# Kernel optimization log

Measured on AMD Instinct MI355X. Metric: run time of the kernel, lower is better.

## Reference

```python
import jax, jax.numpy as jnp
import numpy as np

HEADS = 8
CHANNELS = 256
RR = 1
DH = CHANNELS // RR                 # per-head channels
ATT = HEADS * DH                    # 2048
# exact scale from the torch module
SCALE = (1.0 / np.sqrt(CHANNELS // RR)) / np.sqrt(2.0 / (CHANNELS + 3 * ATT)) * np.sqrt(2.0 / (CHANNELS + ATT))


def setup_inputs() -> dict:
    key = jax.random.key(0)
    k1, k2, k3, k4, k5 = jax.random.split(key, 5)
    x = jax.random.normal(k1, (8, CHANNELS, 32, 32), dtype=jnp.float32)
    # 1x1 conv weights stored as [out_ch, in_ch]
    w_in = jax.random.normal(k2, (3 * ATT, CHANNELS), dtype=jnp.float32) * (1.0 / np.sqrt(CHANNELS))
    b_in = jax.random.normal(k3, (3 * ATT,), dtype=jnp.float32) * 0.02
    w_out = jax.random.normal(k4, (CHANNELS, ATT), dtype=jnp.float32) * (1.0 / np.sqrt(ATT))
    b_out = jax.random.normal(k5, (CHANNELS,), dtype=jnp.float32) * 0.02
    return {"x": x, "w_in": w_in, "b_in": b_in, "w_out": w_out, "b_out": b_out}


def reference(x, w_in, b_in, w_out, b_out):
    n, c, h, w = x.shape
    L = h * w
    xf = x.reshape(n, c, L)
    # 1x1 conv in = channel-mixing matmul, then fixed scale
    scaled = (jnp.einsum('ncl,oc->nol', xf, w_in) + b_in[:, None]) * jnp.float32(SCALE)
    s = scaled.reshape(n, HEADS, 3 * DH, L)
    q, k, v = s[:, :, :DH], s[:, :, DH:2 * DH], s[:, :, 2 * DH:]   # each (n, H, DH, L)
    att = jnp.einsum('nhdl,nhdm->nhlm', q, k)                       # (n, H, L, L)
    # softmax over the FLATTENED L*L axis (global per head), as in the torch code
    att = jax.nn.softmax(att.reshape(n, HEADS, L * L), axis=2).reshape(n, HEADS, L, L)
    out = jnp.einsum('nhdl,nhlm->nhdm', v, att)                     # (n, H, DH, L)
    out = out.reshape(n, ATT, L)
    out = jnp.einsum('nal,ca->ncl', out, w_out) + b_out[:, None]
    return out.reshape(n, c, h, w)
```

## Files before the change

### kernel.cpp

```cpp
#include <hip/hip_runtime.h>
#include <hip/hip_bf16.h>


typedef __bf16 bf16x8 __attribute__((ext_vector_type(8)));
typedef __bf16 bf16x4 __attribute__((ext_vector_type(4)));
typedef float f32x4 __attribute__((ext_vector_type(4)));
typedef __hip_bfloat16 bf16;

__device__ __forceinline__ void async_copy16(const void* g, void* s) {
    __builtin_amdgcn_global_load_lds(
        (const __attribute__((address_space(1))) unsigned int*)g,
        (__attribute__((address_space(3))) unsigned int*)s, 16, 0, 0);
}

__device__ __forceinline__ bf16x8 scale8(bf16x8 v, float s) {
    bf16x8 r;
#pragma unroll
    for (int e = 0; e < 8; ++e) r[e] = (__bf16)((float)v[e] * s);
    return r;
}

__global__ __launch_bounds__(256)
void gemm_nt(const bf16* __restrict__ A, const bf16* __restrict__ B, void* __restrict__ Cvoid,
             int M, int N, int K, int lda, int ldb, int ldc,
             long asn, long ash, long bsn, long bsh, long csn, long csh,
             int H, int mode, const float* __restrict__ bias, const float* __restrict__ Zp,
             float scale)
{
    __shared__ __align__(16) bf16 smem[17408];
    bf16* Alds = smem;
    bf16* Blds = smem + 8192;

    const int tid  = threadIdx.x;
    const int wave = tid >> 6;
    const int lane = tid & 63;
    const int z  = blockIdx.z;
    const int zn = z / H, zh = z % H;

    const bf16* Ab = A + zn * asn + zh * ash;
    const bf16* Bb = B + zn * bsn + zh * bsh;

    const long tM = (long)blockIdx.y * 128;
    const long tN = (long)blockIdx.x * 128;

    const int wr   = (wave >> 1) * 64;
    const int wc   = (wave & 1) * 64;
    const int l15  = lane & 15;
    const int quad = lane >> 4;

    f32x4 acc[4][4] = {};

    const int kiters = K >> 6;
    const bool regB = (mode == 4);

#pragma unroll
    for (int i = 0; i < 4; ++i) {
        const int flat = i * 256 + tid;
        const int row  = flat >> 3;
        const int kcs  = (flat & 7) ^ (row & 7);
        async_copy16(Ab + (tM + row) * (long)lda + kcs * 8,
                     (char*)Alds + (long)(i * 256 + wave * 64) * 16);
        if (!regB) {
            async_copy16(Bb + (tN + row) * (long)ldb + kcs * 8,
                         (char*)Blds + (long)(i * 256 + wave * 64) * 16);
        }
    }
    if (regB) {
        const float zi0 = 1.0f / Zp[zn * 8];
#pragma unroll
        for (int i = 0; i < 4; ++i) {
            const int flat = i * 256 + tid;
            const int row  = flat >> 3;
            const int kcs  = (flat & 7) ^ (row & 7);
            bf16x8 b = *(const bf16x8*)(Bb + (tN + row) * (long)ldb + kcs * 8);
            *(bf16x8*)((char*)Blds + (long)flat * 16) = scale8(b, zi0);
        }
    }

    bf16x8 pfA[4], pfB[4];
    for (int kt = 0; kt < kiters; ++kt) {
        __syncthreads();
        const bool has_next = (kt + 1 < kiters);
        float zin = 1.0f;
        if (has_next) {
            const long kof = (long)(kt + 1) * 64;
            if (regB) zin = 1.0f / Zp[zn * 8 + ((kt + 1) >> 2)];
#pragma unroll
            for (int i = 0; i < 4; ++i) {
                const int flat = i * 256 + tid;
                const int row  = flat >> 3;
                const int kcs  = (flat & 7) ^ (row & 7);
                pfA[i] = *(const bf16x8*)(Ab + (tM + row) * (long)lda + kof + kcs * 8);
                pfB[i] = *(const bf16x8*)(Bb + (tN + row) * (long)ldb + kof + kcs * 8);
            }
        }
#pragma unroll
        for (int kk = 0; kk < 2; ++kk) {
            bf16x8 af[4], bfv[4];
#pragma unroll
            for (int i = 0; i < 4; ++i) {
                const int r = wr + i * 16 + l15;
                af[i] = *(const bf16x8*)(Alds + r * 64 + ((kk * 4 + quad) ^ (r & 7)) * 8);
            }
#pragma unroll
            for (int j = 0; j < 4; ++j) {
                const int r = wc + j * 16 + l15;
                bfv[j] = *(const bf16x8*)(Blds + r * 64 + ((kk * 4 + quad) ^ (r & 7)) * 8);
            }
#pragma unroll
            for (int i = 0; i < 4; ++i)
#pragma unroll
                for (int j = 0; j < 4; ++j)
                    acc[i][j] = __builtin_amdgcn_mfma_f32_16x16x32_bf16(af[i], bfv[j], acc[i][j], 0, 0, 0);
        }
        if (has_next) {
            __builtin_amdgcn_sched_barrier(0);
            __builtin_amdgcn_s_barrier();
            __builtin_amdgcn_sched_barrier(0);
#pragma unroll
            for (int i = 0; i < 4; ++i) {
                const int flat = i * 256 + tid;
                *(bf16x8*)((char*)Alds + (long)flat * 16) = pfA[i];
                *(bf16x8*)((char*)Blds + (long)flat * 16) = regB ? scale8(pfB[i], zin) : pfB[i];
            }
        }
    }

    if (mode >= 3) {
        float* C = (float*)Cvoid + zn * csn + zh * csh;
#pragma unroll
        for (int i = 0; i < 4; ++i)
#pragma unroll
            for (int j = 0; j < 4; ++j)
#pragma unroll
                for (int r = 0; r < 4; ++r) {
                    const long row = tM + wr + i * 16 + quad * 4 + r;
                    const long col = tN + wc + j * 16 + l15;
                    C[row * (long)ldc + col] = acc[i][j][r] + bias[row];
                }
    } else {
        bf16* Cb = (bf16*)Cvoid + zn * csn + zh * csh + tM * (long)ldc + tN;
        __syncthreads();
#pragma unroll
        for (int i = 0; i < 4; ++i)
#pragma unroll
            for (int j = 0; j < 4; ++j)
#pragma unroll
                for (int r = 0; r < 4; ++r) {
                    const int row = wr + i * 16 + quad * 4 + r;
                    const int col = wc + j * 16 + l15;
                    smem[row * 136 + col] = __float2bfloat16((acc[i][j][r] + bias[col]) * scale);
                }
        __syncthreads();
#pragma unroll
        for (int k = 0; k < 8; ++k) {
            const int fc  = k * 256 + tid;
            const int row = fc >> 4, cc = fc & 15;
            const f32x4 val = *(const f32x4*)((const char*)smem + row * 272 + cc * 16);
            *(f32x4*)((char*)(Cb + (long)row * ldc) + cc * 16) = val;
        }
    }
}

__global__ __launch_bounds__(256, 2)
void attn_fused(const bf16* __restrict__ scaled_t, const bf16* __restrict__ v2,
                bf16* __restrict__ out_tt, float* __restrict__ Z)
{
    __shared__ __align__(16) bf16 smem[36880];
    bf16* Ks = smem;
    bf16* Qs = smem + 16384;
    bf16* Ps = smem + 32768;
    float* Zs = (float*)(smem + 36864);

    const int tid  = threadIdx.x;
    const int wave = tid >> 6, lane = tid & 63;
    const int l15  = lane & 15, quad = lane >> 4;

    const int b   = blockIdx.x;
    const int xcd = b & 7, s = b >> 3;
    const int nh  = xcd * 8 + (s >> 4);
    const int mt  = s & 15;
    const int n   = nh >> 3, h = nh & 7;
    const long m0 = (long)mt * 64;

    const bf16* Qb = scaled_t + (long)n * 6291456 + h * 768;
    const bf16* Kb = Qb + 256;
    const bf16* Vb = v2 + (long)nh * 262144;

    f32x4 accO[16] = {};
    float zsum = 0.0f;

#pragma unroll
    for (int i = 0; i < 8; ++i) {
        const int flat = i * 256 + tid;
        const int row  = flat >> 5;
        const int ch   = flat & 31;
        const int kcs  = (ch & 24) | ((ch & 7) ^ (row & 7));
        async_copy16(Kb + (m0 + row) * 6144 + kcs * 8,
                     (char*)Ks + (long)(i * 256 + wave * 64) * 16);
    }
    {
        bf16x8 q0[8];
#pragma unroll
        for (int i = 0; i < 8; ++i) {
            const int flat = i * 256 + tid;
            const int row  = flat >> 5;
            const int ch   = flat & 31;
            const int kcs  = (ch & 24) | ((ch & 7) ^ (row & 7));
            q0[i] = *(const bf16x8*)(Qb + (long)row * 6144 + kcs * 8);
        }
#pragma unroll
        for (int i = 0; i < 8; ++i)
            *(bf16x8*)((char*)Qs + (long)(i * 256 + tid) * 16) = q0[i];
    }
    __syncthreads();

    bf16x8 pfV[8], pfQ[8];
    for (int lt = 0; lt < 16; ++lt) {
        const long l0 = (long)lt * 64;

#pragma unroll
        for (int i = 0; i < 8; ++i) {
            const int flat = i * 256 + tid;
            const int d    = flat >> 3;
            const int kcs  = (flat & 7) ^ (d & 7);
            pfV[i] = *(const bf16x8*)(Vb + (long)d * 1024 + l0 + kcs * 8);
        }

        f32x4 accS[4] = {};
        const int qrow = wave * 16 + l15;
#pragma unroll
        for (int w = 0; w < 8; ++w) {
            const int cw = w * 4 + quad;
            const bf16x8 af = *(const bf16x8*)(
                Qs + qrow * 256 + ((cw & 24) | ((cw & 7) ^ (qrow & 7))) * 8);
#pragma unroll
            for (int j = 0; j < 4; ++j) {
                const int krow = j * 16 + l15;
                const bf16x8 bfv = *(const bf16x8*)(
                    Ks + krow * 256 + ((cw & 24) | ((cw & 7) ^ (krow & 7))) * 8);
                accS[j] = __builtin_amdgcn_mfma_f32_16x16x32_bf16(af, bfv, accS[j], 0, 0, 0);
            }
        }
        {
            const int lbase = wave * 16 + quad * 4;
            const int chunk = lbase >> 3;
#pragma unroll
            for (int j = 0; j < 4; ++j) {
                const int m = j * 16 + l15;
                float e0 = __expf(accS[j][0]);
                float e1 = __expf(accS[j][1]);
                float e2 = __expf(accS[j][2]);
                float e3 = __expf(accS[j][3]);
                zsum += (e0 + e1) + (e2 + e3);
                bf16x4 pk;
                pk[0] = (__bf16)e0; pk[1] = (__bf16)e1; pk[2] = (__bf16)e2; pk[3] = (__bf16)e3;
                *(bf16x4*)(Ps + m * 64 + (chunk ^ (m & 7)) * 8 + (lbase & 7)) = pk;
            }
        }
        __builtin_amdgcn_sched_barrier(0);
        __builtin_amdgcn_s_barrier();
        __builtin_amdgcn_sched_barrier(0);
#pragma unroll
        for (int i = 0; i < 8; ++i)
            *(bf16x8*)((char*)Qs + (long)(i * 256 + tid) * 16) = pfV[i];
        __syncthreads();

        if (lt < 15) {
            const long l0n = l0 + 64;
#pragma unroll
            for (int i = 0; i < 8; ++i) {
                const int flat = i * 256 + tid;
                const int row  = flat >> 5;
                const int ch   = flat & 31;
                const int kcs  = (ch & 24) | ((ch & 7) ^ (row & 7));
                pfQ[i] = *(const bf16x8*)(Qb + (l0n + row) * 6144 + kcs * 8);
            }
        }

        const int mrow = wave * 16 + l15;
#pragma unroll
        for (int w = 0; w < 2; ++w) {
            const int cw = w * 4 + quad;
            const bf16x8 af = *(const bf16x8*)(Ps + mrow * 64 + (cw ^ (mrow & 7)) * 8);
#pragma unroll
            for (int j = 0; j < 16; ++j) {
                const int d = j * 16 + l15;
                const bf16x8 bfv = *(const bf16x8*)(Qs + d * 64 + (cw ^ (d & 7)) * 8);
                accO[j] = __builtin_amdgcn_mfma_f32_16x16x32_bf16(af, bfv, accO[j], 0, 0, 0);
            }
        }
        __builtin_amdgcn_sched_barrier(0);
        __builtin_amdgcn_s_barrier();
        __builtin_amdgcn_sched_barrier(0);
        if (lt < 15) {
#pragma unroll
            for (int i = 0; i < 8; ++i)
                *(bf16x8*)((char*)Qs + (long)(i * 256 + tid) * 16) = pfQ[i];
        }
        __syncthreads();
    }

#pragma unroll
    for (int o = 32; o > 0; o >>= 1) zsum += __shfl_down(zsum, o);
    if (lane == 0) Zs[wave] = zsum;
    __syncthreads();
    if (tid == 0) atomicAdd(Z + nh, (Zs[0] + Zs[1]) + (Zs[2] + Zs[3]));

    bf16* Cs = smem + 16384;
#pragma unroll
    for (int j = 0; j < 16; ++j)
#pragma unroll
        for (int r = 0; r < 4; ++r) {
            const int row = wave * 16 + quad * 4 + r;
            const int col = j * 16 + l15;
            Cs[row * 264 + col] = __float2bfloat16(accO[j][r]);
        }
    __syncthreads();
    bf16* Ob = out_tt + (long)n * 2097152 + m0 * 2048 + h * 256;
#pragma unroll
    for (int k = 0; k < 8; ++k) {
        const int flat = k * 256 + tid;
        const int row  = flat >> 5;
        const int cc   = flat & 31;
        const f32x4 val = *(const f32x4*)((const char*)Cs + (row * 264 + cc * 8) * 2);
        *(f32x4*)((char*)(Ob + (long)row * 2048) + cc * 16) = val;
    }
}

__global__ void prep_convert(const float* __restrict__ w_in, const float* __restrict__ w_out,
                             bf16* __restrict__ w_in_b, bf16* __restrict__ w_out_b,
                             float* __restrict__ Z)
{
    const long gid = (long)blockIdx.x * 256 + threadIdx.x;
    if (blockIdx.x == 0 && threadIdx.x < 64) Z[threadIdx.x] = 0.0f;
    const long n1 = 6144L * 256;
    const long n2 = 256L * 2048;
    const long stride = (long)gridDim.x * 256;
    for (long i = gid; i < n1; i += stride) w_in_b[i] = __float2bfloat16(w_in[i]);
    for (long i = gid; i < n2; i += stride) w_out_b[i] = __float2bfloat16(w_out[i]);
}

__global__ void prep_xt(const float* __restrict__ x, bf16* __restrict__ x_t)
{
    __shared__ float tile[64][65];
    const int b = blockIdx.x;
    const int n = blockIdx.y;
    const int ct = b & 3, lt = b >> 2;
    const int t = threadIdx.x;
    const float* xp = x + (long)n * 256 * 1024;
#pragma unroll
    for (int i = 0; i < 16; ++i) {
        const int flat = i * 256 + t;
        const int cl = flat >> 6, ll = flat & 63;
        tile[cl][ll] = xp[(long)(ct * 64 + cl) * 1024 + lt * 64 + ll];
    }
    __syncthreads();
    bf16* xo = x_t + (long)n * 1024 * 256;
#pragma unroll
    for (int i = 0; i < 16; ++i) {
        const int flat = i * 256 + t;
        const int lr = flat >> 6, cr = flat & 63;
        xo[(long)(lt * 64 + lr) * 256 + ct * 64 + cr] = __float2bfloat16(tile[cr][lr]);
    }
}

__global__ void prep_v2(const bf16* __restrict__ scaled_t, bf16* __restrict__ v2)
{
    __shared__ bf16 tile[64][74];
    const int b  = blockIdx.x;
    const int nh = blockIdx.y;
    const int dt = b & 3, lt = b >> 2;
    const int n = nh >> 3, h = nh & 7;
    const int t = threadIdx.x;
    const bf16* sp = scaled_t + (long)n * 1024 * 6144 + h * 768 + 512;
#pragma unroll
    for (int i = 0; i < 16; ++i) {
        const int flat = i * 256 + t;
        const int lr = flat >> 6, dc = flat & 63;
        tile[dc][lr] = sp[(long)(lt * 64 + lr) * 6144 + dt * 64 + dc];
    }
    __syncthreads();
    bf16* vp = v2 + ((long)nh * 256 + dt * 64) * 1024;
#pragma unroll
    for (int i = 0; i < 16; ++i) {
        const int flat = i * 256 + t;
        const int dr = flat >> 6, lc = flat & 63;
        vp[(long)dr * 1024 + lt * 64 + lc] = tile[dr][lc];
    }
}

extern "C" void kernel_launch(void* const* d_in, const int* in_sizes, int n_in,
                              void* d_out, int out_size, void* d_ws, size_t ws_size,
                              hipStream_t stream)
{
    const float* x     = (const float*)d_in[0];
    const float* w_in  = (const float*)d_in[1];
    const float* b_in  = (const float*)d_in[2];
    const float* w_out = (const float*)d_in[3];
    const float* b_out = (const float*)d_in[4];
    float* out = (float*)d_out;

    const float SCALE = 0.10416666666666667f;

    char* p = (char*)d_ws;
    bf16* scaled_t = (bf16*)p;  p += 100663296;
    bf16* v2       = (bf16*)p;  p += 33554432;
    bf16* out_tt   = (bf16*)p;  p += 33554432;
    bf16* x_t      = (bf16*)p;  p += 4194304;
    bf16* w_in_b   = (bf16*)p;  p += 3145728;
    bf16* w_out_b  = (bf16*)p;  p += 1048576;
    float* Z       = (float*)p; p += 256;

    prep_convert<<<2048, 256, 0, stream>>>(w_in, w_out, w_in_b, w_out_b, Z);
    prep_xt<<<dim3(64, 8), 256, 0, stream>>>(x, x_t);

    gemm_nt<<<dim3(48, 8, 8), 256, 0, stream>>>(
        x_t, w_in_b, scaled_t,
        1024, 6144, 256, 256, 256, 6144,
        1024L * 256, 0, 0, 0, 1024L * 6144, 0,
        1, 0, b_in, nullptr, SCALE);

    prep_v2<<<dim3(64, 64), 256, 0, stream>>>(scaled_t, v2);

    attn_fused<<<1024, 256, 0, stream>>>(scaled_t, v2, out_tt, Z);

    gemm_nt<<<dim3(8, 2, 8), 256, 0, stream>>>(
        w_out_b, out_tt, out,
        256, 1024, 2048, 2048, 2048, 1024,
        0, 0, 1024L * 2048, 0, 256L * 1024, 0,
        1, 4, b_out, Z, 1.0f);
}
```

Measured before the change: 262.0 us.

## Keep Q/K fragments in registers and switch attention to 32x32x16 MFMA

```diff
diff --git a/kernel.cpp b/kernel.cpp
--- a/kernel.cpp
+++ b/kernel.cpp
@@ -5,6 +5,7 @@
 typedef __bf16 bf16x8 __attribute__((ext_vector_type(8)));
 typedef __bf16 bf16x4 __attribute__((ext_vector_type(4)));
 typedef float f32x4 __attribute__((ext_vector_type(4)));
+typedef float f32x16 __attribute__((ext_vector_type(16)));
 typedef __hip_bfloat16 bf16;
 
 __device__ __forceinline__ void async_copy16(const void* g, void* s) {
@@ -166,165 +167,145 @@
 void attn_fused(const bf16* __restrict__ scaled_t, const bf16* __restrict__ v2,
                 bf16* __restrict__ out_tt, float* __restrict__ Z)
 {
-    __shared__ __align__(16) bf16 smem[36880];
-    bf16* Ks = smem;
-    bf16* Qs = smem + 16384;
-    bf16* Ps = smem + 32768;
-    float* Zs = (float*)(smem + 36864);
+    __shared__ __align__(16) bf16 smem[20752];
+    bf16* Vs = smem;
+    bf16* Ps = smem + 16384;
+    float* Zs = (float*)(smem + 20736);
 
     const int tid  = threadIdx.x;
     const int wave = tid >> 6, lane = tid & 63;
-    const int l15  = lane & 15, quad = lane >> 4;
+    const int l31  = lane & 31, hw = lane >> 5;
 
     const int b   = blockIdx.x;
     const int xcd = b & 7, s = b >> 3;
     const int nh  = xcd * 8 + (s >> 4);
-    const int mt  = s & 15;
+    const int mt_ = s & 15;
     const int n   = nh >> 3, h = nh & 7;
-    const long m0 = (long)mt * 64;
+    const long m0 = (long)mt_ * 64;
 
     const bf16* Qb = scaled_t + (long)n * 6291456 + h * 768;
     const bf16* Kb = Qb + 256;
     const bf16* Vb = v2 + (long)nh * 262144;
 
-    f32x4 accO[16] = {};
+    const int wl = wave & 1;
+    const int wm = wave >> 1;
+
+    bf16x8 Kf[16];
+    {
+        const bf16* Krow = Kb + (m0 + wm * 32 + l31) * 6144;
+#pragma unroll
+        for (int w = 0; w < 16; ++w)
+            Kf[w] = *(const bf16x8*)(Krow + w * 16 + hw * 8);
+    }
+
+    const bf16* Qrow = Qb + (wl * 32 + l31) * 6144;
+    bf16x8 Qf[16];
+#pragma unroll
+    for (int w = 0; w < 16; ++w)
+        Qf[w] = *(const bf16x8*)(Qrow + w * 16 + hw * 8);
+
+    f32x16 accO[2][2] = {};
     float zsum = 0.0f;
 
-#pragma unroll
-    for (int i = 0; i < 8; ++i) {
-        const int flat = i * 256 + tid;
-        const int row  = flat >> 5;
-        const int ch   = flat & 31;
-        const int kcs  = (ch & 24) | ((ch & 7) ^ (row & 7));
-        async_copy16(Kb + (m0 + row) * 6144 + kcs * 8,
-                     (char*)Ks + (long)(i * 256 + wave * 64) * 16);
-    }
-    {
-        bf16x8 q0[8];
-#pragma unroll
-        for (int i = 0; i < 8; ++i) {
-            const int flat = i * 256 + tid;
-            const int row  = flat >> 5;
-            const int ch   = flat & 31;
-            const int kcs  = (ch & 24) | ((ch & 7) ^ (row & 7));
-            q0[i] = *(const bf16x8*)(Qb + (long)row * 6144 + kcs * 8);
-        }
-#pragma unroll
-        for (int i = 0; i < 8; ++i)
-            *(bf16x8*)((char*)Qs + (long)(i * 256 + tid) * 16) = q0[i];
-    }
-    __syncthreads();
-
-    bf16x8 pfV[8], pfQ[8];
     for (int lt = 0; lt < 16; ++lt) {
         const long l0 = (long)lt * 64;
+
+        __builtin_amdgcn_sched_barrier(0);
+        __builtin_amdgcn_s_barrier();
+        __builtin_amdgcn_sched_barrier(0);
 
 #pragma unroll
         for (int i = 0; i < 8; ++i) {
             const int flat = i * 256 + tid;
             const int d    = flat >> 3;
-            const int kcs  = (flat & 7) ^ (d & 7);
-            pfV[i] = *(const bf16x8*)(Vb + (long)d * 1024 + l0 + kcs * 8);
-        }
-
-        f32x4 accS[4] = {};
-        const int qrow = wave * 16 + l15;
-#pragma unroll
-        for (int w = 0; w < 8; ++w) {
-            const int cw = w * 4 + quad;
-            const bf16x8 af = *(const bf16x8*)(
-                Qs + qrow * 256 + ((cw & 24) | ((cw & 7) ^ (qrow & 7))) * 8);
-#pragma unroll
-            for (int j = 0; j < 4; ++j) {
-                const int krow = j * 16 + l15;
-                const bf16x8 bfv = *(const bf16x8*)(
-                    Ks + krow * 256 + ((cw & 24) | ((cw & 7) ^ (krow & 7))) * 8);
-                accS[j] = __builtin_amdgcn_mfma_f32_16x16x32_bf16(af, bfv, accS[j], 0, 0, 0);
-            }
-        }
+            const int ch   = flat & 7;
+            async_copy16(Vb + (long)d * 1024 + l0 + ((ch ^ (d & 7)) * 8),
+                         (char*)Vs + (long)(i * 256 + wave * 64) * 16);
+        }
+
+        f32x16 accS = {};
+#pragma unroll
+        for (int w = 0; w < 16; ++w)
+            accS = __builtin_amdgcn_mfma_f32_32x32x16_bf16(Qf[w], Kf[w], accS, 0, 0, 0);
+
         {
-            const int lbase = wave * 16 + quad * 4;
-            const int chunk = lbase >> 3;
-#pragma unroll
-            for (int j = 0; j < 4; ++j) {
-                const int m = j * 16 + l15;
-                float e0 = __expf(accS[j][0]);
-                float e1 = __expf(accS[j][1]);
-                float e2 = __expf(accS[j][2]);
-                float e3 = __expf(accS[j][3]);
-                zsum += (e0 + e1) + (e2 + e3);
+            bf16* prow = Ps + (wm * 32 + l31) * 68 + wl * 32 + 4 * hw;
+#pragma unroll
+            for (int g = 0; g < 4; ++g) {
                 bf16x4 pk;
-                pk[0] = (__bf16)e0; pk[1] = (__bf16)e1; pk[2] = (__bf16)e2; pk[3] = (__bf16)e3;
-                *(bf16x4*)(Ps + m * 64 + (chunk ^ (m & 7)) * 8 + (lbase & 7)) = pk;
-            }
-        }
-        __builtin_amdgcn_sched_barrier(0);
-        __builtin_amdgcn_s_barrier();
-        __builtin_amdgcn_sched_barrier(0);
-#pragma unroll
-        for (int i = 0; i < 8; ++i)
-            *(bf16x8*)((char*)Qs + (long)(i * 256 + tid) * 16) = pfV[i];
+#pragma unroll
+                for (int e = 0; e < 4; ++e) {
+                    const float v = __expf(accS[g * 4 + e]);
+                    zsum += v;
+                    pk[e] = (__bf16)v;
+                }
+                *(bf16x4*)(prow + 8 * g) = pk;
+            }
+        }
+
         __syncthreads();
 
         if (lt < 15) {
-            const long l0n = l0 + 64;
-#pragma unroll
-            for (int i = 0; i < 8; ++i) {
-                const int flat = i * 256 + tid;
-                const int row  = flat >> 5;
-                const int ch   = flat & 31;
-                const int kcs  = (ch & 24) | ((ch & 7) ^ (row & 7));
-                pfQ[i] = *(const bf16x8*)(Qb + (l0n + row) * 6144 + kcs * 8);
-            }
-        }
-
-        const int mrow = wave * 16 + l15;
-#pragma unroll
-        for (int w = 0; w < 2; ++w) {
-            const int cw = w * 4 + quad;
-            const bf16x8 af = *(const bf16x8*)(Ps + mrow * 64 + (cw ^ (mrow & 7)) * 8);
-#pragma unroll
-            for (int j = 0; j < 16; ++j) {
-                const int d = j * 16 + l15;
-                const bf16x8 bfv = *(const bf16x8*)(Qs + d * 64 + (cw ^ (d & 7)) * 8);
-                accO[j] = __builtin_amdgcn_mfma_f32_16x16x32_bf16(af, bfv, accO[j], 0, 0, 0);
-            }
-        }
-        __builtin_amdgcn_sched_barrier(0);
-        __builtin_amdgcn_s_barrier();
-        __builtin_amdgcn_sched_barrier(0);
-        if (lt < 15) {
-#pragma unroll
-            for (int i = 0; i < 8; ++i)
-                *(bf16x8*)((char*)Qs + (long)(i * 256 + tid) * 16) = pfQ[i];
-        }
-        __syncthreads();
-    }
+            const bf16* Qn = Qrow + (l0 + 64) * 6144;
+#pragma unroll
+            for (int w = 0; w < 16; ++w)
+                Qf[w] = *(const bf16x8*)(Qn + w * 16 + hw * 8);
+        }
+
+#pragma unroll
+        for (int kw = 0; kw < 4; ++kw) {
+            bf16x8 pf[2], vf[2];
+#pragma unroll
+            for (int mt = 0; mt < 2; ++mt) {
+                const bf16* pp = Ps + (mt * 32 + l31) * 68 + kw * 16 + hw * 8;
+                const bf16x4 lo = *(const bf16x4*)pp;
+                const bf16x4 hi = *(const bf16x4*)(pp + 4);
+#pragma unroll
+                for (int e = 0; e < 4; ++e) { pf[mt][e] = lo[e]; pf[mt][4 + e] = hi[e]; }
+            }
+#pragma unroll
+            for (int dt = 0; dt < 2; ++dt) {
+                const int d    = wave * 64 + dt * 32 + l31;
+                const int slot = (kw * 2 + hw) ^ (d & 7);
+                vf[dt] = *(const bf16x8*)(Vs + d * 64 + slot * 8);
+            }
+#pragma unroll
+            for (int mt = 0; mt < 2; ++mt)
+#pragma unroll
+                for (int dt = 0; dt < 2; ++dt)
+                    accO[mt][dt] = __builtin_amdgcn_mfma_f32_32x32x16_bf16(
+                        pf[mt], vf[dt], accO[mt][dt], 0, 0, 0);
+        }
+    }
+
+    __syncthreads();
 
 #pragma unroll
     for (int o = 32; o > 0; o >>= 1) zsum += __shfl_down(zsum, o);
     if (lane == 0) Zs[wave] = zsum;
+
+    bf16* Cs = smem;
+#pragma unroll
+    for (int mt = 0; mt < 2; ++mt)
+#pragma unroll
+        for (int dt = 0; dt < 2; ++dt)
+#pragma unroll
+            for (int r = 0; r < 16; ++r) {
+                const int m = mt * 32 + (r & 3) + 8 * (r >> 2) + 4 * hw;
+                const int d = wave * 64 + dt * 32 + l31;
+                Cs[m * 264 + d] = __float2bfloat16(accO[mt][dt][r]);
+            }
     __syncthreads();
     if (tid == 0) atomicAdd(Z + nh, (Zs[0] + Zs[1]) + (Zs[2] + Zs[3]));
 
-    bf16* Cs = smem + 16384;
-#pragma unroll
-    for (int j = 0; j < 16; ++j)
-#pragma unroll
-        for (int r = 0; r < 4; ++r) {
-            const int row = wave * 16 + quad * 4 + r;
-            const int col = j * 16 + l15;
-            Cs[row * 264 + col] = __float2bfloat16(accO[j][r]);
-        }
-    __syncthreads();
     bf16* Ob = out_tt + (long)n * 2097152 + m0 * 2048 + h * 256;
 #pragma unroll
     for (int k = 0; k < 8; ++k) {
         const int flat = k * 256 + tid;
         const int row  = flat >> 5;
-        const int cc   = flat & 31;
-        const f32x4 val = *(const f32x4*)((const char*)Cs + (row * 264 + cc * 8) * 2);
-        *(f32x4*)((char*)(Ob + (long)row * 2048) + cc * 16) = val;
+        const int c    = flat & 31;
+        const f32x4 val = *(const f32x4*)((const char*)Cs + row * 528 + c * 16);
+        *(f32x4*)((char*)(Ob + (long)row * 2048) + c * 16) = val;
     }
 }
 
```

After: 319.3 us. +21.8%, slower.
